# Performance work log

Hardware: AMD Instinct MI355X
Metric: run time of the kernel (lower is better)

The kernel has to match this reference:

```python
import jax, jax.numpy as jnp
import numpy as np

M, H = 7, 200                 # ensemble size, hidden width
OBS, ACT = 32, 8
C = OBS + ACT                 # model input dim
DOUT = OBS + 1                # next-obs delta + reward
N = 100000                    # number of transitions
E_NUM = 5                     # number of elites
MAX_LOGVAR, MIN_LOGVAR = 0.5, -10.0
REWARD_SCALE, REWARD_BIAS = 1.0, 0.0
TERM_THRESH = 50.0


def setup_inputs() -> dict:
    key = jax.random.key(0)
    ks = jax.random.split(key, 10)
    def w(k, shape, fan_in):
        return jax.random.normal(k, shape, jnp.float32) / np.float32(np.sqrt(fan_in))
    return {
        "observations": jax.random.normal(ks[0], (N, OBS), jnp.float32),
        "actions": jax.random.normal(ks[1], (N, ACT), jnp.float32),
        "scaler_mu": jax.random.normal(ks[2], (C,), jnp.float32) * 0.1,
        "scaler_std": jax.random.uniform(ks[3], (C,), jnp.float32, 0.5, 1.5),
        "W1": w(ks[4], (M, C, H), C), "b1": jnp.zeros((M, 1, H), jnp.float32),
        "W2": w(ks[5], (M, H, H), H), "b2": jnp.zeros((M, 1, H), jnp.float32),
        "W3": w(ks[6], (M, H, H), H), "b3": jnp.zeros((M, 1, H), jnp.float32),
        "W4": w(ks[7], (M, H, 2 * DOUT), H), "b4": jnp.zeros((M, 1, 2 * DOUT), jnp.float32),
        "elites": jnp.arange(E_NUM, dtype=jnp.int32),
    }


def _ensemble_mlp(z, W1, b1, W2, b2, W3, b3, W4, b4):
    # z: [M, R, C] -> mean, logvar: [M, R, DOUT]
    h = jax.nn.swish(jnp.einsum('mrc,mch->mrh', z, W1) + b1)
    h = jax.nn.swish(jnp.einsum('mrh,mhk->mrk', h, W2) + b2)
    h = jax.nn.swish(jnp.einsum('mrh,mhk->mrk', h, W3) + b3)
    out = jnp.einsum('mrh,mhk->mrk', h, W4) + b4
    mean, logvar = out[..., :DOUT], out[..., DOUT:]
    logvar = MAX_LOGVAR - jax.nn.softplus(MAX_LOGVAR - logvar)
    logvar = MIN_LOGVAR + jax.nn.softplus(logvar - MIN_LOGVAR)
    return mean, logvar


def _terminal_fn(observations, actions, next_obs):
    # simple environment-style terminal predicate, shape [N, 1]
    return jnp.linalg.norm(next_obs, axis=-1, keepdims=True) > TERM_THRESH


def reference(observations, actions, scaler_mu, scaler_std,
              W1, b1, W2, b2, W3, b3, W4, b4, elites):
    key = jax.random.key(0)  # source uses the SAME key for permutation and noise
    z = jnp.concatenate([observations, actions], axis=1)
    z = (z - scaler_mu) / scaler_std
    n, c = z.shape
    e = elites.shape[0]
    r = (n - 1) // e + 1
    pad = e * r - n
    z = jnp.concatenate([z, jnp.zeros((pad, c), z.dtype)], axis=0)
    idxs = jax.random.permutation(key, e * r)
    tmp = z[idxs].reshape(e, r, c)                    # dispatch to elite slots
    zf = jnp.zeros((M, r, c), z.dtype).at[elites].set(tmp)
    mean, logvar = _ensemble_mlp(zf, W1, b1, W2, b2, W3, b3, W4, b4)
    std = jnp.exp(0.5 * logvar)
    ensemble_samples = mean + jax.random.normal(key, mean.shape) * std
    res = ensemble_samples[elites].reshape(e * r, DOUT)   # gather elites back
    es = jnp.zeros((e * r, DOUT), res.dtype).at[idxs].set(res)[:n]  # inverse perm
    samples = jnp.concatenate([es[:, :-1] + observations, es[:, -1:]], axis=1)
    next_obs = samples[..., :-1]
    reward = samples[..., -1] * REWARD_SCALE + REWARD_BIAS
    terminal = _terminal_fn(observations, actions, next_obs).squeeze(1)
    return next_obs, reward, terminal
```

## Files before the change

kernel.cpp:

```cpp
#include <hip/hip_runtime.h>
#include <stdint.h>

#define N_TOT   100000
#define NPAD    100352
#define NBLK    98
#define HISTN   (256 * NBLK)
#define R_PER   20000
#define NOISE_HALF 2310000u
#define PERM_HALF  50000u

#define JAX_PARTITIONABLE 1

#define ROWS 32
#define RG_N 2
#define BPM  625
#define MLP_GRID (5 * BPM)
#define KST  200

#define L1_U4 1664
#define L2_U4 5824
#define L4_U4 2240
#define PM_U4 (L1_U4 + 2 * L2_U4 + L4_U4)
#define L1OFF 0
#define L2OFF L1_U4
#define L3OFF (L1_U4 + L2_U4)
#define L4OFF (L1_U4 + 2 * L2_U4)
#define WPACK_BLOCKS 304

using f32x4  = __attribute__((ext_vector_type(4))) float;
using bf16x8 = __attribute__((ext_vector_type(8))) short;

__host__ __device__ __forceinline__ uint32_t rotl32(uint32_t x, unsigned d) {
  return (x << d) | (x >> (32u - d));
}

__host__ __device__ inline void tf2x32(uint32_t k0, uint32_t k1,
                                       uint32_t x0, uint32_t x1,
                                       uint32_t& o0, uint32_t& o1) {
  uint32_t k2 = k0 ^ k1 ^ 0x1BD11BDAu;
  x0 += k0; x1 += k1;
#define TFR(R) { x0 += x1; x1 = rotl32(x1, R); x1 ^= x0; }
  TFR(13u) TFR(15u) TFR(26u) TFR(6u)
  x0 += k1; x1 += k2 + 1u;
  TFR(17u) TFR(29u) TFR(16u) TFR(24u)
  x0 += k2; x1 += k0 + 2u;
  TFR(13u) TFR(15u) TFR(26u) TFR(6u)
  x0 += k0; x1 += k1 + 3u;
  TFR(17u) TFR(29u) TFR(16u) TFR(24u)
  x0 += k1; x1 += k2 + 4u;
  TFR(13u) TFR(15u) TFR(26u) TFR(6u)
  x0 += k2; x1 += k0 + 5u;
#undef TFR
  o0 = x0; o1 = x1;
}

__host__ __device__ inline uint32_t jax_bits32(uint32_t k0, uint32_t k1,
                                               uint32_t idx, uint32_t half) {
#if JAX_PARTITIONABLE
  (void)half;
  uint32_t o0, o1; tf2x32(k0, k1, 0u, idx, o0, o1);
  return o0 ^ o1;
#else
  uint32_t o0, o1;
  if (idx < half) { tf2x32(k0, k1, idx, idx + half, o0, o1); return o0; }
  else            { tf2x32(k0, k1, idx - half, idx, o0, o1); return o1; }
#endif
}

static void jax_split_host(uint32_t k0, uint32_t k1,
                           uint32_t* nk, uint32_t* sk) {
#if JAX_PARTITIONABLE
  tf2x32(k0, k1, 0u, 0u, nk[0], nk[1]);
  tf2x32(k0, k1, 0u, 1u, sk[0], sk[1]);
#else
  uint32_t a0, a1, b0, b1;
  tf2x32(k0, k1, 0u, 2u, a0, a1);
  tf2x32(k0, k1, 1u, 3u, b0, b1);
  nk[0] = a0; nk[1] = b0;
  sk[0] = a1; sk[1] = b1;
#endif
}

__device__ __forceinline__ void split2(float e0, float e1,
                                       uint32_t& hi, uint32_t& lo) {
  uint32_t u0 = __float_as_uint(e0), u1 = __float_as_uint(e1);
  float f0 = __uint_as_float(u0 & 0xFFFF0000u);
  float f1 = __uint_as_float(u1 & 0xFFFF0000u);
  uint32_t l0 = __float_as_uint(e0 - f0) >> 16;
  uint32_t l1 = __float_as_uint(e1 - f1) >> 16;
  hi = (u1 & 0xFFFF0000u) | (u0 >> 16);
  lo = (l1 << 16) | l0;
}

__device__ __forceinline__ void split1(float x, unsigned short& h,
                                       unsigned short& l) {
  uint32_t u = __float_as_uint(x);
  float fh = __uint_as_float(u & 0xFFFF0000u);
  h = (unsigned short)(u >> 16);
  l = (unsigned short)(__float_as_uint(x - fh) >> 16);
}

__device__ __forceinline__ float rec1(unsigned short h, unsigned short l) {
  return __uint_as_float((uint32_t)h << 16) + __uint_as_float((uint32_t)l << 16);
}

__device__ __forceinline__ bf16x8 punu4(uint4 x) {
  union { uint4 u; bf16x8 v; } t;
  t.u = x;
  return t.v;
}

__global__ __launch_bounds__(256) void k_pre(uint32_t kk0, uint32_t kk1,
                                             uint32_t* __restrict__ keys,
                                             uint32_t* __restrict__ vals,
                                             uint32_t* __restrict__ hist,
                                             uint32_t* __restrict__ histZ,
                                             const float* __restrict__ W1,
                                             const float* __restrict__ W2,
                                             const float* __restrict__ W3,
                                             const float* __restrict__ W4,
                                             uint4* __restrict__ wpH,
                                             uint4* __restrict__ wpL) {
  __shared__ uint32_t h[256];
  int tid = threadIdx.x;
  if (blockIdx.x < NBLK) {
    int b = blockIdx.x;
    h[tid] = 0;
    __syncthreads();
    uint32_t base = b * 1024u + tid * 4u;
    uint32_t kq[4], vq[4];
#pragma unroll
    for (int j = 0; j < 4; ++j) {
      uint32_t i = base + j;
      if (i < (uint32_t)N_TOT) {
        kq[j] = jax_bits32(kk0, kk1, i, PERM_HALF);
        vq[j] = i;
      } else {
        kq[j] = 0xFFFFFFFFu;
        vq[j] = 0xFFFFFFFFu;
      }
      atomicAdd(&h[kq[j] & 255u], 1u);
    }
    *(uint4*)(keys + base) = make_uint4(kq[0], kq[1], kq[2], kq[3]);
    *(uint4*)(vals + base) = make_uint4(vq[0], vq[1], vq[2], vq[3]);
    __syncthreads();
    hist[tid * NBLK + b] = h[tid];
    histZ[tid * NBLK + b] = 0;
  } else {
    int flat = (blockIdx.x - NBLK) * 256 + tid;
    if (flat >= 5 * PM_U4) return;
    int m = flat / PM_U4;
    int rem = flat - m * PM_U4;
    const float* W; int KIN, KOUT, nch, loc;
    if (rem < L2OFF)      { W = W1 + (size_t)m * 40 * 200;  KIN = 40;  KOUT = 200; nch = 2; loc = rem; }
    else if (rem < L3OFF) { W = W2 + (size_t)m * 200 * 200; KIN = 200; KOUT = 200; nch = 7; loc = rem - L2OFF; }
    else if (rem < L4OFF) { W = W3 + (size_t)m * 200 * 200; KIN = 200; KOUT = 200; nch = 7; loc = rem - L3OFF; }
    else                  { W = W4 + (size_t)m * 200 * 66;  KIN = 200; KOUT = 66;  nch = 7; loc = rem - L4OFF; }
    int lane = loc & 63;
    int tc = loc >> 6;
    int ch = tc % nch;
    int t  = tc / nch;
    int g = lane >> 4, cr = lane & 15;
    int k0 = ch * 32 + g * 8;
    int col = t * 16 + cr;
    const bool ok = (k0 < KIN) && (col < KOUT);
    float w[8];
#pragma unroll
    for (int j = 0; j < 8; ++j)
      w[j] = ok ? W[(size_t)(k0 + j) * KOUT + col] : 0.f;
    uint32_t hi[4], lo[4];
#pragma unroll
    for (int d = 0; d < 4; ++d)
      split2(w[2 * d], w[2 * d + 1], hi[d], lo[d]);
    wpH[flat] = make_uint4(hi[0], hi[1], hi[2], hi[3]);
    wpL[flat] = make_uint4(lo[0], lo[1], lo[2], lo[3]);
  }
}

template<bool GENNEXT, bool LAST>
__global__ __launch_bounds__(1024) void k_scat(const uint32_t* __restrict__ keyIn,
                                               const uint32_t* __restrict__ valIn,
                                               uint32_t* __restrict__ keyOut,
                                               uint32_t* __restrict__ valOut,
                                               const uint32_t* __restrict__ histRaw,
                                               uint32_t* __restrict__ histNext,
                                               uint32_t* __restrict__ histZero,
                                               int shift, uint32_t nk0, uint32_t nk1) {
  __shared__ __align__(16) uint8_t blob[HISTN * 4];
  __shared__ uint32_t tot[256];
  __shared__ uint32_t bas[256];
  __shared__ uint32_t bef[256];
  __shared__ uint32_t offD[256];
  const int b = blockIdx.x, tid = threadIdx.x;

  const uint32_t key = keyIn[b * 1024 + tid];
  const uint32_t val = valIn[b * 1024 + tid];

  {
    uint32_t* ldsH = (uint32_t*)blob;
    for (int x = tid; x < HISTN; x += 1024) ldsH[x] = histRaw[x];
    __syncthreads();
    if (tid < 256) {
      uint32_t before = 0, t = 0;
      for (int b2 = 0; b2 < NBLK; ++b2) {
        uint32_t v2 = ldsH[tid * NBLK + b2];
        before += (b2 < b) ? v2 : 0u;
        t += v2;
      }
      tot[tid] = t; bef[tid] = before; bas[tid] = t;
    }
    __syncthreads();
    for (int off = 1; off < 256; off <<= 1) {
      uint32_t v = 0;
      if (tid < 256 && tid >= off) v = bas[tid - off];
      __syncthreads();
      if (tid < 256) bas[tid] += v;
      __syncthreads();
    }
    if (tid < 256) offD[tid] = bas[tid] - tot[tid] + bef[tid];
    __syncthreads();
  }

  uint32_t* dig   = (uint32_t*)blob;
  uint32_t* histc = (uint32_t*)(blob + 4096);
  const uint32_t d = (key >> shift) & 255u;
  const int cp = tid >> 6;
  for (int x = tid; x < 16 * 256; x += 1024) histc[x] = 0;
  __syncthreads();
  dig[tid] = d;
  atomicAdd(&histc[cp * 256 + d], 1u);
  __syncthreads();
  if (tid < 256) {
    uint32_t run = 0;
#pragma unroll
    for (int c = 0; c < 16; ++c) {
      uint32_t t = histc[c * 256 + tid];
      histc[c * 256 + tid] = run;
      run += t;
    }
  }
  __syncthreads();
  int c = 0;
  for (int p = cp * 64; p < tid; ++p)
    c += (dig[p] == d);
  const uint32_t rank = histc[cp * 256 + d] + (uint32_t)c;
  const uint32_t off = offD[d] + rank;
  valOut[off] = val;
  if (!LAST) {
    uint32_t nkey;
    int nshift;
    if (GENNEXT) {
      nkey = (off < (uint32_t)N_TOT) ? jax_bits32(nk0, nk1, off, PERM_HALF)
                                     : 0xFFFFFFFFu;
      nshift = 0;
    } else {
      nkey = key;
      nshift = shift + 8;
    }
    keyOut[off] = nkey;
    atomicAdd(&histNext[((nkey >> nshift) & 255u) * NBLK + (off >> 10)], 1u);
    if (tid < 256) histZero[b * 256 + tid] = 0;
  }
}

__device__ inline float softplusf(float x) {
  float ax = fabsf(x);
  float r = log1pf(expf(-ax));
  return (x > 0.f) ? x + r : r;
}

__device__ inline float erfinvf_approx(float x) {
  float w = -logf((1.0f - x) * (1.0f + x));
  float p;
  if (w < 5.0f) {
    w = w - 2.5f;
    p = 2.81022636e-08f;
    p = fmaf(p, w, 3.43273939e-07f);
    p = fmaf(p, w, -3.5233877e-06f);
    p = fmaf(p, w, -4.39150654e-06f);
    p = fmaf(p, w, 0.00021858087f);
    p = fmaf(p, w, -0.00125372503f);
    p = fmaf(p, w, -0.00417768164f);
    p = fmaf(p, w, 0.246640727f);
    p = fmaf(p, w, 1.50140941f);
  } else {
    w = sqrtf(w) - 3.0f;
    p = -0.000200214257f;
    p = fmaf(p, w, 0.000100950558f);
    p = fmaf(p, w, 0.00134934322f);
    p = fmaf(p, w, -0.00367342844f);
    p = fmaf(p, w, 0.00573950773f);
    p = fmaf(p, w, -0.0076224613f);
    p = fmaf(p, w, 0.00943887047f);
    p = fmaf(p, w, 1.00167406f);
    p = fmaf(p, w, 2.83297682f);
  }
  return p * x;
}

template<int KOUT, int NTILES, int NCH, bool ACTV>
__device__ __forceinline__ void layer_mfma(unsigned short* __restrict__ Ahi,
                                           unsigned short* __restrict__ Alo,
                                           const uint4* __restrict__ wpH,
                                           const uint4* __restrict__ wpL,
                                           int woff,
                                           const float* __restrict__ bm,
                                           int wv, int lane) {
  constexpr int MAXT = (NTILES + 3) / 4;
  const int g  = lane >> 4;
  const int cr = lane & 15;
  f32x4 acc[RG_N][MAXT];
#pragma unroll
  for (int rg = 0; rg < RG_N; ++rg)
#pragma unroll
    for (int ti = 0; ti < MAXT; ++ti)
      acc[rg][ti] = (f32x4){0.f, 0.f, 0.f, 0.f};

  for (int ch = 0; ch < NCH; ++ch) {
    const int k0 = ch * 32 + g * 8;
    const bool ok = (k0 + 8 <= KST);
    const int ka = ok ? k0 : 0;
    uint4 hfa[RG_N], lfa[RG_N];
#pragma unroll
    for (int rg = 0; rg < RG_N; ++rg) {
      uint4 h = *(const uint4*)(Ahi + (rg * 16 + cr) * KST + ka);
      uint4 l = *(const uint4*)(Alo + (rg * 16 + cr) * KST + ka);
      if (!ok) { h = make_uint4(0, 0, 0, 0); l = make_uint4(0, 0, 0, 0); }
      hfa[rg] = h; lfa[rg] = l;
    }
#pragma unroll
    for (int ti = 0; ti < MAXT; ++ti) {
      const int t = wv + ti * 4;
      if (t < NTILES) {
        const int idx = woff + (t * NCH + ch) * 64 + lane;
        bf16x8 vbh = punu4(wpH[idx]);
        bf16x8 vbl = punu4(wpL[idx]);
#pragma unroll
        for (int rg = 0; rg < RG_N; ++rg) {
          bf16x8 vah = punu4(hfa[rg]);
          bf16x8 val = punu4(lfa[rg]);
          acc[rg][ti] = __builtin_amdgcn_mfma_f32_16x16x32_bf16(vah, vbh, acc[rg][ti], 0, 0, 0);
          acc[rg][ti] = __builtin_amdgcn_mfma_f32_16x16x32_bf16(val, vbh, acc[rg][ti], 0, 0, 0);
          acc[rg][ti] = __builtin_amdgcn_mfma_f32_16x16x32_bf16(vah, vbl, acc[rg][ti], 0, 0, 0);
        }
      }
    }
  }
  __syncthreads();
#pragma unroll
  for (int ti = 0; ti < MAXT; ++ti) {
    const int t = wv + ti * 4;
    if (t < NTILES) {
      const int col = t * 16 + cr;
      if (col < KOUT) {
        const float bias = bm[col];
#pragma unroll
        for (int rg = 0; rg < RG_N; ++rg) {
#pragma unroll
          for (int rr = 0; rr < 4; ++rr) {
            float x = acc[rg][ti][rr] + bias;
            if (ACTV) x = x / (1.0f + expf(-x));
            unsigned short h, l;
            split1(x, h, l);
            const int row = rg * 16 + g * 4 + rr;
            Ahi[row * KST + col] = h;
            Alo[row * KST + col] = l;
          }
        }
      }
    }
  }
  __syncthreads();
}

__global__ __launch_bounds__(256, 6) void k_mlp(
    const float* __restrict__ obs, const float* __restrict__ act,
    const float* __restrict__ mu, const float* __restrict__ sst,
    const uint4* __restrict__ wpH, const uint4* __restrict__ wpL,
    const float* __restrict__ b1, const float* __restrict__ b2,
    const float* __restrict__ b3, const float* __restrict__ b4,
    const uint32_t* __restrict__ idxs, float* __restrict__ outv) {
  __shared__ __align__(16) unsigned short Ahi[ROWS * KST];
  __shared__ __align__(16) unsigned short Alo[ROWS * KST];
  __shared__ uint32_t jrow[ROWS];
  __shared__ float nrm[ROWS];
  __shared__ float muv[40];
  __shared__ float rsd[40];
  const int tid = threadIdx.x;
  const int m  = blockIdx.x / BPM;
  const int bb = blockIdx.x - m * BPM;
  const int i0 = m * R_PER + bb * ROWS;
  const int wv = tid >> 6;
  const int lane = tid & 63;
  const int mw = m * PM_U4;

  if (tid < ROWS) {
    jrow[tid] = idxs[i0 + tid];
    nrm[tid] = 0.f;
  }
  if (tid >= 64 && tid < 104) {
    int cc = tid - 64;
    muv[cc] = mu[cc];
    rsd[cc] = 1.0f / sst[cc];
  }
  __syncthreads();

  for (int t = tid; t < ROWS * 64; t += 256) {
    int rr = t >> 6, cc = t & 63;
    float v = 0.f;
    if (cc < 40) {
      uint32_t j = jrow[rr];
      float x = (cc < 32) ? obs[(size_t)j * 32 + cc] : act[(size_t)j * 8 + (cc - 32)];
      v = (x - muv[cc]) * rsd[cc];
    }
    unsigned short h, l;
    split1(v, h, l);
    Ahi[rr * KST + cc] = h;
    Alo[rr * KST + cc] = l;
  }
  __syncthreads();

  layer_mfma<200, 13, 2, true >(Ahi, Alo, wpH, wpL, mw + L1OFF, b1 + (size_t)m * 200, wv, lane);
  layer_mfma<200, 13, 7, true >(Ahi, Alo, wpH, wpL, mw + L2OFF, b2 + (size_t)m * 200, wv, lane);
  layer_mfma<200, 13, 7, true >(Ahi, Alo, wpH, wpL, mw + L3OFF, b3 + (size_t)m * 200, wv, lane);
  layer_mfma< 66,  5, 7, false>(Ahi, Alo, wpH, wpL, mw + L4OFF, b4 + (size_t)m * 66, wv, lane);

  float* onext = outv;
  float* orew  = outv + 3200000;
  float* oterm = outv + 3300000;

  for (int t = tid; t < ROWS * 33; t += 256) {
    int rw = t / 33, kc = t - rw * 33;
    float mean = rec1(Ahi[rw * KST + kc],      Alo[rw * KST + kc]);
    float lvr  = rec1(Ahi[rw * KST + 33 + kc], Alo[rw * KST + 33 + kc]);
    float lv = 0.5f - softplusf(0.5f - lvr);
    lv = -10.0f + softplusf(lv + 10.0f);
    float sd = expf(0.5f * lv);
    int q = bb * ROWS + rw;
    uint32_t tno = (uint32_t)(m * 660000 + q * 33 + kc);
    uint32_t bits = jax_bits32(0u, 0u, tno, NOISE_HALF);
    float f = __uint_as_float((bits >> 9) | 0x3F800000u) - 1.0f;
    const float LOu = -0.99999994f;
    float u = fmaxf(LOu, fmaf(f, 2.0f, LOu));
    float nz = 1.41421356237f * erfinvf_approx(u);
    float s = mean + nz * sd;
    uint32_t j = jrow[rw];
    if (kc < 32) {
      float no = s + obs[(size_t)j * 32 + kc];
      onext[(size_t)j * 32 + kc] = no;
      atomicAdd(&nrm[rw], no * no);
    } else {
      orew[j] = s;
    }
  }
  __syncthreads();
  if (tid < ROWS) {
    uint32_t j = jrow[tid];
    oterm[j] = (sqrtf(nrm[tid]) > 50.0f) ? 1.0f : 0.0f;
  }
}

extern "C" void kernel_launch(void* const* d_in, const int* in_sizes, int n_in,
                              void* d_out, int out_size, void* d_ws, size_t ws_size,
                              hipStream_t stream) {
  (void)in_sizes; (void)n_in; (void)out_size; (void)ws_size;
  const float* obs = (const float*)d_in[0];
  const float* act = (const float*)d_in[1];
  const float* mu  = (const float*)d_in[2];
  const float* sst = (const float*)d_in[3];
  const float* W1  = (const float*)d_in[4];
  const float* b1  = (const float*)d_in[5];
  const float* W2  = (const float*)d_in[6];
  const float* b2  = (const float*)d_in[7];
  const float* W3  = (const float*)d_in[8];
  const float* b3  = (const float*)d_in[9];
  const float* W4  = (const float*)d_in[10];
  const float* b4  = (const float*)d_in[11];

  uint8_t* ws = (uint8_t*)d_ws;
  uint32_t* keysA = (uint32_t*)(ws);
  uint32_t* keysB = (uint32_t*)(ws + 401408);
  uint32_t* valsA = (uint32_t*)(ws + 802816);
  uint32_t* valsB = (uint32_t*)(ws + 1204224);
  uint32_t* hA    = (uint32_t*)(ws + 1605632);
  uint32_t* hB    = (uint32_t*)(ws + 1705984);
  uint32_t* hC    = (uint32_t*)(ws + 1806336);
  uint4*    wpH   = (uint4*)(ws + 1906688);
  uint4*    wpL   = (uint4*)(ws + 3150848);

  uint32_t key0[2] = {0u, 0u}, key1[2], sub1[2], key2[2], sub2[2];
  jax_split_host(key0[0], key0[1], key1, sub1);
  jax_split_host(key1[0], key1[1], key2, sub2);

  dim3 g(NBLK), blk(256), blk1k(1024);

  k_pre<<<dim3(NBLK + WPACK_BLOCKS), blk, 0, stream>>>(sub1[0], sub1[1],
      keysA, valsA, hA, hB, W1, W2, W3, W4, wpH, wpL);
  k_scat<false,false><<<g, blk1k, 0, stream>>>(keysA, valsA, keysB, valsB, hA, hB, hC, 0,  0u, 0u);
  k_scat<false,false><<<g, blk1k, 0, stream>>>(keysB, valsB, keysA, valsA, hB, hC, hA, 8,  0u, 0u);
  k_scat<false,false><<<g, blk1k, 0, stream>>>(keysA, valsA, keysB, valsB, hC, hA, hB, 16, 0u, 0u);
  k_scat<true, false><<<g, blk1k, 0, stream>>>(keysB, valsB, keysA, valsA, hA, hB, hC, 24, sub2[0], sub2[1]);
  k_scat<false,false><<<g, blk1k, 0, stream>>>(keysA, valsA, keysB, valsB, hB, hC, hA, 0,  0u, 0u);
  k_scat<false,false><<<g, blk1k, 0, stream>>>(keysB, valsB, keysA, valsA, hC, hA, hB, 8,  0u, 0u);
  k_scat<false,false><<<g, blk1k, 0, stream>>>(keysA, valsA, keysB, valsB, hA, hB, hC, 16, 0u, 0u);
  k_scat<false,true ><<<g, blk1k, 0, stream>>>(keysB, valsB, keysA, valsA, hB, hC, hA, 24, 0u, 0u);

  k_mlp<<<dim3(MLP_GRID), blk, 0, stream>>>(obs, act, mu, sst,
                                            wpH, wpL, b1, b2, b3, b4,
                                            valsA, (float*)d_out);
}
```

Measured before the change: 307.3 us.

## Fuse eight radix-sort scatter passes into one cooperative kernel with grid sync

```diff
diff --git a/kernel.cpp b/kernel.cpp
--- a/kernel.cpp
+++ b/kernel.cpp
@@ -1,5 +1,8 @@
 #include <hip/hip_runtime.h>
+#include <hip/hip_cooperative_groups.h>
 #include <stdint.h>
+
+namespace cg = cooperative_groups;
 
 #define N_TOT   100000
 #define NPAD    100352
@@ -177,89 +180,105 @@
   }
 }
 
-template<bool GENNEXT, bool LAST>
-__global__ __launch_bounds__(1024) void k_scat(const uint32_t* __restrict__ keyIn,
-                                               const uint32_t* __restrict__ valIn,
-                                               uint32_t* __restrict__ keyOut,
-                                               uint32_t* __restrict__ valOut,
-                                               const uint32_t* __restrict__ histRaw,
-                                               uint32_t* __restrict__ histNext,
-                                               uint32_t* __restrict__ histZero,
-                                               int shift, uint32_t nk0, uint32_t nk1) {
+__global__ __launch_bounds__(1024) void k_sort8(uint32_t* kA, uint32_t* kB,
+                                                uint32_t* vA, uint32_t* vB,
+                                                uint32_t* h0, uint32_t* h1,
+                                                uint32_t* h2,
+                                                uint32_t nk0, uint32_t nk1) {
+  cg::grid_group grid = cg::this_grid();
   __shared__ __align__(16) uint8_t blob[HISTN * 4];
   __shared__ uint32_t tot[256];
   __shared__ uint32_t bas[256];
   __shared__ uint32_t bef[256];
   __shared__ uint32_t offD[256];
   const int b = blockIdx.x, tid = threadIdx.x;
-
-  const uint32_t key = keyIn[b * 1024 + tid];
-  const uint32_t val = valIn[b * 1024 + tid];
-
-  {
-    uint32_t* ldsH = (uint32_t*)blob;
-    for (int x = tid; x < HISTN; x += 1024) ldsH[x] = histRaw[x];
+  uint32_t* hs[3] = {h0, h1, h2};
+
+  for (int p = 0; p < 8; ++p) {
+    const uint32_t* keyIn  = (p & 1) ? kB : kA;
+    const uint32_t* valIn  = (p & 1) ? vB : vA;
+    uint32_t*       keyOut = (p & 1) ? kA : kB;
+    uint32_t*       valOut = (p & 1) ? vA : vB;
+    const uint32_t* histRaw  = hs[p % 3];
+    uint32_t*       histNext = hs[(p + 1) % 3];
+    uint32_t*       histZero = hs[(p + 2) % 3];
+    const int  shift = (8 * p) & 31;
+    const bool gen  = (p == 3);
+    const bool last = (p == 7);
+
+    const uint32_t key = keyIn[b * 1024 + tid];
+    const uint32_t val = valIn[b * 1024 + tid];
+
+    {
+      uint32_t* ldsH = (uint32_t*)blob;
+      for (int x = tid; x < HISTN; x += 1024) ldsH[x] = histRaw[x];
+      __syncthreads();
+      if (tid < 256) {
+        uint32_t before = 0, t = 0;
+        for (int b2 = 0; b2 < NBLK; ++b2) {
+          uint32_t v2 = ldsH[tid * NBLK + b2];
+          before += (b2 < b) ? v2 : 0u;
+          t += v2;
+        }
+        tot[tid] = t; bef[tid] = before; bas[tid] = t;
+      }
+      __syncthreads();
+      for (int off = 1; off < 256; off <<= 1) {
+        uint32_t v = 0;
+        if (tid < 256 && tid >= off) v = bas[tid - off];
+        __syncthreads();
+        if (tid < 256) bas[tid] += v;
+        __syncthreads();
+      }
+      if (tid < 256) offD[tid] = bas[tid] - tot[tid] + bef[tid];
+      __syncthreads();
+    }
+
+    uint32_t* dig   = (uint32_t*)blob;
+    uint32_t* histc = (uint32_t*)(blob + 4096);
+    const uint32_t d = (key >> shift) & 255u;
+    const int cp = tid >> 6;
+    for (int x = tid; x < 16 * 256; x += 1024) histc[x] = 0;
+    __syncthreads();
+    dig[tid] = d;
+    atomicAdd(&histc[cp * 256 + d], 1u);
     __syncthreads();
     if (tid < 256) {
-      uint32_t before = 0, t = 0;
-      for (int b2 = 0; b2 < NBLK; ++b2) {
-        uint32_t v2 = ldsH[tid * NBLK + b2];
-        before += (b2 < b) ? v2 : 0u;
-        t += v2;
-      }
-      tot[tid] = t; bef[tid] = before; bas[tid] = t;
+      uint32_t run = 0;
+#pragma unroll
+      for (int c = 0; c < 16; ++c) {
+        uint32_t t = histc[c * 256 + tid];
+        histc[c * 256 + tid] = run;
+        run += t;
+      }
     }
     __syncthreads();
-    for (int off = 1; off < 256; off <<= 1) {
-      uint32_t v = 0;
-      if (tid < 256 && tid >= off) v = bas[tid - off];
+    int c = 0;
+    for (int q = cp * 64; q < tid; ++q)
+      c += (dig[q] == d);
+    const uint32_t rank = histc[cp * 256 + d] + (uint32_t)c;
+    const uint32_t off = offD[d] + rank;
+    valOut[off] = val;
+    if (!last) {
+      uint32_t nkey;
+      int nshift;
+      if (gen) {
+        nkey = (off < (uint32_t)N_TOT) ? jax_bits32(nk0, nk1, off, PERM_HALF)
+                                       : 0xFFFFFFFFu;
+        nshift = 0;
+      } else {
+        nkey = key;
+        nshift = shift + 8;
+      }
+      keyOut[off] = nkey;
+      atomicAdd(&histNext[((nkey >> nshift) & 255u) * NBLK + (off >> 10)], 1u);
+      if (tid < 256) histZero[b * 256 + tid] = 0;
+    }
+    if (p < 7) {
+      __threadfence();
       __syncthreads();
-      if (tid < 256) bas[tid] += v;
-      __syncthreads();
-    }
-    if (tid < 256) offD[tid] = bas[tid] - tot[tid] + bef[tid];
-    __syncthreads();
-  }
-
-  uint32_t* dig   = (uint32_t*)blob;
-  uint32_t* histc = (uint32_t*)(blob + 4096);
-  const uint32_t d = (key >> shift) & 255u;
-  const int cp = tid >> 6;
-  for (int x = tid; x < 16 * 256; x += 1024) histc[x] = 0;
-  __syncthreads();
-  dig[tid] = d;
-  atomicAdd(&histc[cp * 256 + d], 1u);
-  __syncthreads();
-  if (tid < 256) {
-    uint32_t run = 0;
-#pragma unroll
-    for (int c = 0; c < 16; ++c) {
-      uint32_t t = histc[c * 256 + tid];
-      histc[c * 256 + tid] = run;
-      run += t;
-    }
-  }
-  __syncthreads();
-  int c = 0;
-  for (int p = cp * 64; p < tid; ++p)
-    c += (dig[p] == d);
-  const uint32_t rank = histc[cp * 256 + d] + (uint32_t)c;
-  const uint32_t off = offD[d] + rank;
-  valOut[off] = val;
-  if (!LAST) {
-    uint32_t nkey;
-    int nshift;
-    if (GENNEXT) {
-      nkey = (off < (uint32_t)N_TOT) ? jax_bits32(nk0, nk1, off, PERM_HALF)
-                                     : 0xFFFFFFFFu;
-      nshift = 0;
-    } else {
-      nkey = key;
-      nshift = shift + 8;
-    }
-    keyOut[off] = nkey;
-    atomicAdd(&histNext[((nkey >> nshift) & 255u) * NBLK + (off >> 10)], 1u);
-    if (tid < 256) histZero[b * 256 + tid] = 0;
+      grid.sync();
+    }
   }
 }
 
@@ -492,18 +511,15 @@
   jax_split_host(key0[0], key0[1], key1, sub1);
   jax_split_host(key1[0], key1[1], key2, sub2);
 
-  dim3 g(NBLK), blk(256), blk1k(1024);
+  dim3 blk(256);
 
   k_pre<<<dim3(NBLK + WPACK_BLOCKS), blk, 0, stream>>>(sub1[0], sub1[1],
       keysA, valsA, hA, hB, W1, W2, W3, W4, wpH, wpL);
-  k_scat<false,false><<<g, blk1k, 0, stream>>>(keysA, valsA, keysB, valsB, hA, hB, hC, 0,  0u, 0u);
-  k_scat<false,false><<<g, blk1k, 0, stream>>>(keysB, valsB, keysA, valsA, hB, hC, hA, 8,  0u, 0u);
-  k_scat<false,false><<<g, blk1k, 0, stream>>>(keysA, valsA, keysB, valsB, hC, hA, hB, 16, 0u, 0u);
-  k_scat<true, false><<<g, blk1k, 0, stream>>>(keysB, valsB, keysA, valsA, hA, hB, hC, 24, sub2[0], sub2[1]);
-  k_scat<false,false><<<g, blk1k, 0, stream>>>(keysA, valsA, keysB, valsB, hB, hC, hA, 0,  0u, 0u);
-  k_scat<false,false><<<g, blk1k, 0, stream>>>(keysB, valsB, keysA, valsA, hC, hA, hB, 8,  0u, 0u);
-  k_scat<false,false><<<g, blk1k, 0, stream>>>(keysA, valsA, keysB, valsB, hA, hB, hC, 16, 0u, 0u);
-  k_scat<false,true ><<<g, blk1k, 0, stream>>>(keysB, valsB, keysA, valsA, hB, hC, hA, 24, 0u, 0u);
+
+  uint32_t s20 = sub2[0], s21 = sub2[1];
+  void* args[] = {&keysA, &keysB, &valsA, &valsB, &hA, &hB, &hC, &s20, &s21};
+  hipLaunchCooperativeKernel((const void*)k_sort8, dim3(NBLK), dim3(1024),
+                             args, 0, stream);
 
   k_mlp<<<dim3(MLP_GRID), blk, 0, stream>>>(obs, act, mu, sst,
                                             wpH, wpL, b1, b2, b3, b4,
```

New measurement: 722.7 us. 135% more time.

## Halve radix-sort block size and read block-major histograms directly from global

Applied to the files above, without the earlier changes.

```diff
diff --git a/kernel.cpp b/kernel.cpp
--- a/kernel.cpp
+++ b/kernel.cpp
@@ -3,8 +3,9 @@
 
 #define N_TOT   100000
 #define NPAD    100352
-#define NBLK    98
-#define HISTN   (256 * NBLK)
+#define NBLK    196
+#define EPB     512
+#define HISTN   (NBLK * 256)
 #define R_PER   20000
 #define NOISE_HALF 2310000u
 #define PERM_HALF  50000u
@@ -127,10 +128,10 @@
     int b = blockIdx.x;
     h[tid] = 0;
     __syncthreads();
-    uint32_t base = b * 1024u + tid * 4u;
-    uint32_t kq[4], vq[4];
-#pragma unroll
-    for (int j = 0; j < 4; ++j) {
+    uint32_t base = b * (uint32_t)EPB + tid * 2u;
+    uint32_t kq[2], vq[2];
+#pragma unroll
+    for (int j = 0; j < 2; ++j) {
       uint32_t i = base + j;
       if (i < (uint32_t)N_TOT) {
         kq[j] = jax_bits32(kk0, kk1, i, PERM_HALF);
@@ -141,11 +142,11 @@
       }
       atomicAdd(&h[kq[j] & 255u], 1u);
     }
-    *(uint4*)(keys + base) = make_uint4(kq[0], kq[1], kq[2], kq[3]);
-    *(uint4*)(vals + base) = make_uint4(vq[0], vq[1], vq[2], vq[3]);
+    *(uint2*)(keys + base) = make_uint2(kq[0], kq[1]);
+    *(uint2*)(vals + base) = make_uint2(vq[0], vq[1]);
     __syncthreads();
-    hist[tid * NBLK + b] = h[tid];
-    histZ[tid * NBLK + b] = 0;
+    hist[b * 256 + tid] = h[tid];
+    histZ[b * 256 + tid] = 0;
   } else {
     int flat = (blockIdx.x - NBLK) * 256 + tid;
     if (flat >= 5 * PM_U4) return;
@@ -178,36 +179,43 @@
 }
 
 template<bool GENNEXT, bool LAST>
-__global__ __launch_bounds__(1024) void k_scat(const uint32_t* __restrict__ keyIn,
-                                               const uint32_t* __restrict__ valIn,
-                                               uint32_t* __restrict__ keyOut,
-                                               uint32_t* __restrict__ valOut,
-                                               const uint32_t* __restrict__ histRaw,
-                                               uint32_t* __restrict__ histNext,
-                                               uint32_t* __restrict__ histZero,
-                                               int shift, uint32_t nk0, uint32_t nk1) {
-  __shared__ __align__(16) uint8_t blob[HISTN * 4];
+__global__ __launch_bounds__(512) void k_scat(const uint32_t* __restrict__ keyIn,
+                                              const uint32_t* __restrict__ valIn,
+                                              uint32_t* __restrict__ keyOut,
+                                              uint32_t* __restrict__ valOut,
+                                              const uint32_t* __restrict__ histRaw,
+                                              uint32_t* __restrict__ histNext,
+                                              uint32_t* __restrict__ histZero,
+                                              int shift, uint32_t nk0, uint32_t nk1) {
+  __shared__ uint32_t ptot[2][256];
+  __shared__ uint32_t pbef[2][256];
   __shared__ uint32_t tot[256];
   __shared__ uint32_t bas[256];
-  __shared__ uint32_t bef[256];
   __shared__ uint32_t offD[256];
+  __shared__ uint32_t dig[EPB];
+  __shared__ uint32_t histc[8 * 256];
   const int b = blockIdx.x, tid = threadIdx.x;
 
-  const uint32_t key = keyIn[b * 1024 + tid];
-  const uint32_t val = valIn[b * 1024 + tid];
+  const uint32_t key = keyIn[b * EPB + tid];
+  const uint32_t val = valIn[b * EPB + tid];
 
   {
-    uint32_t* ldsH = (uint32_t*)blob;
-    for (int x = tid; x < HISTN; x += 1024) ldsH[x] = histRaw[x];
+    const int d8 = tid & 255;
+    const int half = tid >> 8;
+    uint32_t t = 0, before = 0;
+    const int b0 = half * (NBLK / 2);
+    for (int b2 = b0; b2 < b0 + NBLK / 2; ++b2) {
+      uint32_t v2 = histRaw[b2 * 256 + d8];
+      t += v2;
+      before += (b2 < b) ? v2 : 0u;
+    }
+    ptot[half][d8] = t;
+    pbef[half][d8] = before;
     __syncthreads();
     if (tid < 256) {
-      uint32_t before = 0, t = 0;
-      for (int b2 = 0; b2 < NBLK; ++b2) {
-        uint32_t v2 = ldsH[tid * NBLK + b2];
-        before += (b2 < b) ? v2 : 0u;
-        t += v2;
-      }
-      tot[tid] = t; bef[tid] = before; bas[tid] = t;
+      uint32_t tt = ptot[0][tid] + ptot[1][tid];
+      tot[tid] = tt;
+      bas[tid] = tt;
     }
     __syncthreads();
     for (int off = 1; off < 256; off <<= 1) {
@@ -217,15 +225,13 @@
       if (tid < 256) bas[tid] += v;
       __syncthreads();
     }
-    if (tid < 256) offD[tid] = bas[tid] - tot[tid] + bef[tid];
-    __syncthreads();
-  }
-
-  uint32_t* dig   = (uint32_t*)blob;
-  uint32_t* histc = (uint32_t*)(blob + 4096);
+    if (tid < 256)
+      offD[tid] = bas[tid] - tot[tid] + pbef[0][tid] + pbef[1][tid];
+  }
+
   const uint32_t d = (key >> shift) & 255u;
   const int cp = tid >> 6;
-  for (int x = tid; x < 16 * 256; x += 1024) histc[x] = 0;
+  for (int x = tid; x < 8 * 256; x += EPB) histc[x] = 0;
   __syncthreads();
   dig[tid] = d;
   atomicAdd(&histc[cp * 256 + d], 1u);
@@ -233,7 +239,7 @@
   if (tid < 256) {
     uint32_t run = 0;
 #pragma unroll
-    for (int c = 0; c < 16; ++c) {
+    for (int c = 0; c < 8; ++c) {
       uint32_t t = histc[c * 256 + tid];
       histc[c * 256 + tid] = run;
       run += t;
@@ -258,7 +264,7 @@
       nshift = shift + 8;
     }
     keyOut[off] = nkey;
-    atomicAdd(&histNext[((nkey >> nshift) & 255u) * NBLK + (off >> 10)], 1u);
+    atomicAdd(&histNext[(off / EPB) * 256 + ((nkey >> nshift) & 255u)], 1u);
     if (tid < 256) histZero[b * 256 + tid] = 0;
   }
 }
@@ -483,27 +489,27 @@
   uint32_t* valsA = (uint32_t*)(ws + 802816);
   uint32_t* valsB = (uint32_t*)(ws + 1204224);
   uint32_t* hA    = (uint32_t*)(ws + 1605632);
-  uint32_t* hB    = (uint32_t*)(ws + 1705984);
-  uint32_t* hC    = (uint32_t*)(ws + 1806336);
-  uint4*    wpH   = (uint4*)(ws + 1906688);
-  uint4*    wpL   = (uint4*)(ws + 3150848);
+  uint32_t* hB    = (uint32_t*)(ws + 1806336);
+  uint32_t* hC    = (uint32_t*)(ws + 2007040);
+  uint4*    wpH   = (uint4*)(ws + 2207744);
+  uint4*    wpL   = (uint4*)(ws + 3451904);
 
   uint32_t key0[2] = {0u, 0u}, key1[2], sub1[2], key2[2], sub2[2];
   jax_split_host(key0[0], key0[1], key1, sub1);
   jax_split_host(key1[0], key1[1], key2, sub2);
 
-  dim3 g(NBLK), blk(256), blk1k(1024);
+  dim3 g(NBLK), blk(256), blk512(512);
 
   k_pre<<<dim3(NBLK + WPACK_BLOCKS), blk, 0, stream>>>(sub1[0], sub1[1],
       keysA, valsA, hA, hB, W1, W2, W3, W4, wpH, wpL);
-  k_scat<false,false><<<g, blk1k, 0, stream>>>(keysA, valsA, keysB, valsB, hA, hB, hC, 0,  0u, 0u);
-  k_scat<false,false><<<g, blk1k, 0, stream>>>(keysB, valsB, keysA, valsA, hB, hC, hA, 8,  0u, 0u);
-  k_scat<false,false><<<g, blk1k, 0, stream>>>(keysA, valsA, keysB, valsB, hC, hA, hB, 16, 0u, 0u);
-  k_scat<true, false><<<g, blk1k, 0, stream>>>(keysB, valsB, keysA, valsA, hA, hB, hC, 24, sub2[0], sub2[1]);
-  k_scat<false,false><<<g, blk1k, 0, stream>>>(keysA, valsA, keysB, valsB, hB, hC, hA, 0,  0u, 0u);
-  k_scat<false,false><<<g, blk1k, 0, stream>>>(keysB, valsB, keysA, valsA, hC, hA, hB, 8,  0u, 0u);
-  k_scat<false,false><<<g, blk1k, 0, stream>>>(keysA, valsA, keysB, valsB, hA, hB, hC, 16, 0u, 0u);
-  k_scat<false,true ><<<g, blk1k, 0, stream>>>(keysB, valsB, keysA, valsA, hB, hC, hA, 24, 0u, 0u);
+  k_scat<false,false><<<g, blk512, 0, stream>>>(keysA, valsA, keysB, valsB, hA, hB, hC, 0,  0u, 0u);
+  k_scat<false,false><<<g, blk512, 0, stream>>>(keysB, valsB, keysA, valsA, hB, hC, hA, 8,  0u, 0u);
+  k_scat<false,false><<<g, blk512, 0, stream>>>(keysA, valsA, keysB, valsB, hC, hA, hB, 16, 0u, 0u);
+  k_scat<true, false><<<g, blk512, 0, stream>>>(keysB, valsB, keysA, valsA, hA, hB, hC, 24, sub2[0], sub2[1]);
+  k_scat<false,false><<<g, blk512, 0, stream>>>(keysA, valsA, keysB, valsB, hB, hC, hA, 0,  0u, 0u);
+  k_scat<false,false><<<g, blk512, 0, stream>>>(keysB, valsB, keysA, valsA, hC, hA, hB, 8,  0u, 0u);
+  k_scat<false,false><<<g, blk512, 0, stream>>>(keysA, valsA, keysB, valsB, hA, hB, hC, 16, 0u, 0u);
+  k_scat<false,true ><<<g, blk512, 0, stream>>>(keysB, valsB, keysA, valsA, hB, hC, hA, 24, 0u, 0u);
 
   k_mlp<<<dim3(MLP_GRID), blk, 0, stream>>>(obs, act, mu, sst,
                                             wpH, wpL, b1, b2, b3, b4,
```

After: 302.4 us. About the same (-1.6%).
